# Kernel tuning notes

Measured on AMD Instinct MI355X. Metric: run time of the kernel, lower is better.

The kernel has to match this reference:

```python
import jax, jax.numpy as jnp
import numpy as np

B, L, H = 2, 2048, 1024
NH = 4
K = int(H * 0.5)       # key_dim = 512
V = int(H * 1.0)       # value_dim = 1024
DK, DV = K // NH, V // NH   # 128, 256
PR = 32                # proj_low_rank_dim
GR = 64                # gate_low_rank_dim
EPS = 1e-5


def setup_inputs() -> dict:
    key = jax.random.key(0)
    ks = jax.random.split(key, 16)
    s = 0.02
    return {
        "x": jax.random.normal(ks[0], (B, L, H), jnp.float32),
        "mu_x": jax.random.normal(ks[1], (H,), jnp.float32) * s,      # LerpLinear mu of x_proj[0]
        "Wx1": jax.random.normal(ks[2], (5 * PR, H), jnp.float32) * s,  # x_proj[0].linear
        "Wx2": jax.random.normal(ks[3], (H, 5 * PR), jnp.float32) * s,  # x_proj[2]
        "x_bias": jax.random.normal(ks[4], (5, H), jnp.float32) * s,
        "Wr": jax.random.normal(ks[5], (K, H), jnp.float32) * s,
        "Wk": jax.random.normal(ks[6], (K, H), jnp.float32) * s,
        "Wv": jax.random.normal(ks[7], (V, H), jnp.float32) * s,
        "Wg": jax.random.normal(ks[8], (V, H), jnp.float32) * s,
        "Ww1": jax.random.normal(ks[9], (GR, H), jnp.float32) * s,     # w_proj LoRA down
        "Ww2": jax.random.normal(ks[10], (K, GR), jnp.float32) * s,    # w_proj LoRA up
        "bw2": jax.random.normal(ks[11], (K,), jnp.float32) * s,
        "bonus": jax.random.normal(ks[12], (NH, DK), jnp.float32) * s,  # u
        "ln_w": jnp.ones((DV,), jnp.float32),
        "ln_b": jnp.zeros((DV,), jnp.float32),
        "Wo": jax.random.normal(ks[13], (H, V), jnp.float32) * s,
    }


def reference(x, mu_x, Wx1, Wx2, x_bias, Wr, Wk, Wv, Wg, Ww1, Ww2, bw2,
              bonus, ln_w, ln_b, Wo):
    b, l, h = x.shape
    # token shift: shifted[t] = x[t-1], zeros at t=0 (nn.ZeroPad2d((0,0,1,-1)))
    shifted = jnp.pad(x, ((0, 0), (1, 0), (0, 0)))[:, :-1]
    delta = shifted - x

    # x_proj: LerpLinear -> tanh -> einsum with o_proj-like weight, 5 mixing vectors
    xp = jnp.tanh((x + delta * mu_x) @ Wx1.T).reshape(b, l, 5, PR)
    mus = jnp.einsum('blnr,hnr->blnh', xp, Wx2.reshape(H, 5, PR)) + x_bias
    mu_r, mu_w, mu_k, mu_v, mu_g = (mus[:, :, i] for i in range(5))

    # DDLerpLinear projections: linear(x + delta * mu)
    r = (x + delta * mu_r) @ Wr.T                                   # [B,L,K]
    w = jnp.tanh((x + delta * mu_w) @ Ww1.T) @ Ww2.T + bw2          # LoRA, [B,L,K]
    k = (x + delta * mu_k) @ Wk.T                                   # [B,L,K]
    v = (x + delta * mu_v) @ Wv.T                                   # [B,L,V]
    g = (x + delta * mu_g) @ Wg.T                                   # [B,L,V]

    r = r.reshape(b, l, NH, DK)
    k = k.reshape(b, l, NH, DK)
    v = v.reshape(b, l, NH, DV)
    w = -jnp.exp(w.reshape(b, l, NH, DK))   # log-decay (negative)

    def step(S, inp):
        r_t, k_t, v_t, w_t = inp                                    # [B,h,dk]/[B,h,dv]
        kv = k_t[..., :, None] * v_t[..., None, :]                  # [B,h,dk,dv]
        o_t = jnp.einsum('bhk,bhkv->bhv', r_t,
                         S + bonus[None, :, :, None] * kv)
        S = jnp.exp(w_t)[..., None] * S + kv
        return S, o_t

    seq = (r.transpose(1, 0, 2, 3), k.transpose(1, 0, 2, 3),
           v.transpose(1, 0, 2, 3), w.transpose(1, 0, 2, 3))
    S0 = jnp.zeros((b, NH, DK, DV), x.dtype)
    _, o = jax.lax.scan(step, S0, seq)       # [L,B,h,dv]
    o = o.transpose(1, 0, 2, 3)              # [B,L,h,dv]

    # per-head LayerNorm fused with swish gate
    mean = o.mean(-1, keepdims=True)
    var = o.var(-1, keepdims=True)
    o = (o - mean) * jax.lax.rsqrt(var + EPS) * ln_w + ln_b
    gh = g.reshape(b, l, NH, DV)
    o = o * (gh * jax.nn.sigmoid(gh))        # swish gate

    return o.reshape(b, l, V) @ Wo.T         # [B,L,H]
```

## Files before the change

### kernel.cpp

```cpp
#include <hip/hip_runtime.h>
#include <cstdint>
#include <cstddef>

#define H     1024
#define LSEQ  2048
#define NHH   4
#define DKK   128
#define DVV   256
#define KDIM  512
#define VDIM  1024
#define GRR   64
#define MTOT  4096

enum { EPI_NONE = 0, EPI_TANH = 1, EPI_DEC = 3 };

typedef __attribute__((ext_vector_type(8))) _Float16 half8;
typedef __attribute__((ext_vector_type(4))) float f32x4;
typedef __attribute__((ext_vector_type(2))) float f32x2;

static __device__ __forceinline__ unsigned short f2h(float f) {
    _Float16 h = (_Float16)f;
    union { _Float16 h; unsigned short u; } c;
    c.h = h;
    return c.u;
}

template<int CTRL>
static __device__ __forceinline__ f32x2 dpp_add2(f32x2 x) {
    int lo = __builtin_amdgcn_update_dpp(0, __float_as_int(x.x), CTRL, 0xf, 0xf, true);
    int hi = __builtin_amdgcn_update_dpp(0, __float_as_int(x.y), CTRL, 0xf, 0xf, true);
    f32x2 m;
    m.x = __int_as_float(lo);
    m.y = __int_as_float(hi);
    return x + m;
}

__global__ __launch_bounds__(256) void lerp5_kernel(
    const float* __restrict__ xp,
    const float* __restrict__ Wx2,
    const float* __restrict__ xb,
    const float* __restrict__ x,
    unsigned short* __restrict__ insb)
{
    __shared__ float As[16][64];
    __shared__ float Bs[16][64];
    const int m0 = blockIdx.x * 64;
    const int n0 = blockIdx.y * 64;
    const int t  = threadIdx.x;
    const int tx = t & 15, ty = t >> 4;
    const int sm = t >> 2;
    const int sq = (t & 3) * 4;
    const int nbase = n0 + tx * 4;

    float4 xv[4], pv[4];
#pragma unroll
    for (int i = 0; i < 4; i++) {
        const int m = m0 + ty * 4 + i;
        xv[i] = *(const float4*)(x + (size_t)m * H + nbase);
        pv[i] = make_float4(0.f, 0.f, 0.f, 0.f);
        if ((m & (LSEQ - 1)) != 0)
            pv[i] = *(const float4*)(x + (size_t)(m - 1) * H + nbase);
    }

    for (int z = 0; z < 5; z++) {
        const int acol = z * 32;
        float acc[4][4];
#pragma unroll
        for (int i = 0; i < 4; i++)
#pragma unroll
            for (int j = 0; j < 4; j++) acc[i][j] = 0.f;

#pragma unroll
        for (int k0 = 0; k0 < 32; k0 += 16) {
            {
                const int m = m0 + sm;
                const float4 av = *(const float4*)(xp + (size_t)m * 256 + acol + k0 + sq);
                As[sq + 0][sm] = av.x; As[sq + 1][sm] = av.y;
                As[sq + 2][sm] = av.z; As[sq + 3][sm] = av.w;
            }
            {
                const int n = n0 + sm;
                const float4 bv = *(const float4*)(Wx2 + (size_t)n * 160 + acol + k0 + sq);
                Bs[sq + 0][sm] = bv.x; Bs[sq + 1][sm] = bv.y;
                Bs[sq + 2][sm] = bv.z; Bs[sq + 3][sm] = bv.w;
            }
            __syncthreads();
#pragma unroll
            for (int kk = 0; kk < 16; kk++) {
                const float4 a = *(const float4*)&As[kk][ty * 4];
                const float4 b = *(const float4*)&Bs[kk][tx * 4];
                const float av2[4] = {a.x, a.y, a.z, a.w};
                const float bv2[4] = {b.x, b.y, b.z, b.w};
#pragma unroll
                for (int i = 0; i < 4; i++)
#pragma unroll
                    for (int j = 0; j < 4; j++) acc[i][j] += av2[i] * bv2[j];
            }
            __syncthreads();
        }

        const float4 bb = *(const float4*)(xb + z * H + nbase);
        unsigned short* dst = insb + (size_t)z * 4194304;
#pragma unroll
        for (int i = 0; i < 4; i++) {
            const int m = m0 + ty * 4 + i;
            float4 r;
            r.x = xv[i].x + (pv[i].x - xv[i].x) * (acc[i][0] + bb.x);
            r.y = xv[i].y + (pv[i].y - xv[i].y) * (acc[i][1] + bb.y);
            r.z = xv[i].z + (pv[i].z - xv[i].z) * (acc[i][2] + bb.z);
            r.w = xv[i].w + (pv[i].w - xv[i].w) * (acc[i][3] + bb.w);
            ushort4 p;
            p.x = f2h(r.x); p.y = f2h(r.y); p.z = f2h(r.z); p.w = f2h(r.w);
            *(ushort4*)(dst + (size_t)m * H + nbase) = p;
        }
    }
}

template<int EPI>
__global__ __launch_bounds__(256) void gemm_mfma_bt(
    const unsigned short* __restrict__ A,
    const unsigned short* __restrict__ A2, int nsplit, int lda,
    const unsigned short* __restrict__ B, int ldb,
    float* __restrict__ C, unsigned short* __restrict__ Ch, int ldc, int K,
    const float* __restrict__ bias)
{
    __shared__ __align__(16) unsigned short As[128 * 32];
    __shared__ __align__(16) unsigned short Bs[128 * 32];
    const int t    = threadIdx.x;
    const int w    = t >> 6;
    const int lane = t & 63;
    const int m0 = blockIdx.x * 128;
    const int n0 = blockIdx.y * 128;
    const unsigned short* Au = (n0 < nsplit) ? A : A2;
    const int mw = (w & 1) * 64;
    const int nw = (w >> 1) * 64;
    const int l15 = lane & 15;
    const int q4  = lane >> 4;

    f32x4 acc[4][4];
#pragma unroll
    for (int i = 0; i < 4; i++)
#pragma unroll
        for (int j = 0; j < 4; j++) {
            f32x4 z = {0.f, 0.f, 0.f, 0.f};
            acc[i][j] = z;
        }

    for (int k0 = 0; k0 < K; k0 += 32) {
        __syncthreads();
#pragma unroll
        for (int jj = 0; jj < 2; jj++) {
            const int c   = w * 128 + jj * 64 + lane;
            const int row = c >> 2;
            const int col = (c & 3) * 8;
            __builtin_amdgcn_global_load_lds(
                (const __attribute__((address_space(1))) void*)(Au + (size_t)(m0 + row) * lda + k0 + col),
                (__attribute__((address_space(3))) void*)((char*)As + (w * 128 + jj * 64) * 16),
                16, 0, 0);
            __builtin_amdgcn_global_load_lds(
                (const __attribute__((address_space(1))) void*)(B + (size_t)(n0 + row) * ldb + k0 + col),
                (__attribute__((address_space(3))) void*)((char*)Bs + (w * 128 + jj * 64) * 16),
                16, 0, 0);
        }
        __syncthreads();

        half8 a[4], b[4];
#pragma unroll
        for (int i = 0; i < 4; i++)
            a[i] = *(const half8*)(As + (mw + i * 16 + l15) * 32 + q4 * 8);
#pragma unroll
        for (int j = 0; j < 4; j++)
            b[j] = *(const half8*)(Bs + (nw + j * 16 + l15) * 32 + q4 * 8);
#pragma unroll
        for (int i = 0; i < 4; i++)
#pragma unroll
            for (int j = 0; j < 4; j++)
                acc[i][j] = __builtin_amdgcn_mfma_f32_16x16x32_f16(a[i], b[j], acc[i][j], 0, 0, 0);
    }

#pragma unroll
    for (int i = 0; i < 4; i++) {
        const int m_base = m0 + mw + i * 16 + q4 * 4;
#pragma unroll
        for (int j = 0; j < 4; j++) {
            const int n = n0 + nw + j * 16 + l15;
#pragma unroll
            for (int r = 0; r < 4; r++) {
                float val = acc[i][j][r];
                if constexpr (EPI == EPI_TANH) {
                    C[(size_t)(m_base + r) * ldc + n] = tanhf(val);
                } else if constexpr (EPI == EPI_DEC) {
                    C[(size_t)(m_base + r) * ldc + n] = expf(-expf(val + bias[n]));
                } else {
                    C[(size_t)(m_base + r) * ldc + n] = val;
                }
            }
        }
    }
}

__global__ __launch_bounds__(256) void gemm_fused3(
    const unsigned short* __restrict__ s0, const unsigned short* __restrict__ s1,
    const unsigned short* __restrict__ s2, const unsigned short* __restrict__ s3,
    const unsigned short* __restrict__ s4,
    const unsigned short* __restrict__ Ww1p, const unsigned short* __restrict__ Wrb,
    const unsigned short* __restrict__ Wvb,
    unsigned short* __restrict__ wlow16, float* __restrict__ rkB,
    float* __restrict__ vgB)
{
    const int y = blockIdx.y;
    const unsigned short *Au, *Bp;
    float* C = nullptr;
    unsigned short* Ch = nullptr;
    int n0, ldc;
    if (y == 0) {
        Au = s1; Bp = Ww1p; n0 = 0; ldc = 128; Ch = wlow16;
    } else if (y <= 8) {
        n0 = (y - 1) * 128;
        Au = (n0 < 512) ? s0 : s2;
        Bp = Wrb; C = rkB; ldc = 1024;
    } else {
        n0 = (y - 9) * 128;
        Au = (n0 < 1024) ? s3 : s4;
        Bp = Wvb; C = vgB; ldc = 2048;
    }

    __shared__ __align__(16) unsigned short As[128 * 32];
    __shared__ __align__(16) unsigned short Bs[128 * 32];
    const int t    = threadIdx.x;
    const int w    = t >> 6;
    const int lane = t & 63;
    const int m0 = blockIdx.x * 128;
    const int mw = (w & 1) * 64;
    const int nw = (w >> 1) * 64;
    const int l15 = lane & 15;
    const int q4  = lane >> 4;

    f32x4 acc[4][4];
#pragma unroll
    for (int i = 0; i < 4; i++)
#pragma unroll
        for (int j = 0; j < 4; j++) {
            f32x4 z = {0.f, 0.f, 0.f, 0.f};
            acc[i][j] = z;
        }

    for (int k0 = 0; k0 < H; k0 += 32) {
        __syncthreads();
#pragma unroll
        for (int jj = 0; jj < 2; jj++) {
            const int c   = w * 128 + jj * 64 + lane;
            const int row = c >> 2;
            const int col = (c & 3) * 8;
            __builtin_amdgcn_global_load_lds(
                (const __attribute__((address_space(1))) void*)(Au + (size_t)(m0 + row) * H + k0 + col),
                (__attribute__((address_space(3))) void*)((char*)As + (w * 128 + jj * 64) * 16),
                16, 0, 0);
            __builtin_amdgcn_global_load_lds(
                (const __attribute__((address_space(1))) void*)(Bp + (size_t)(n0 + row) * H + k0 + col),
                (__attribute__((address_space(3))) void*)((char*)Bs + (w * 128 + jj * 64) * 16),
                16, 0, 0);
        }
        __syncthreads();

        half8 a[4], b[4];
#pragma unroll
        for (int i = 0; i < 4; i++)
            a[i] = *(const half8*)(As + (mw + i * 16 + l15) * 32 + q4 * 8);
#pragma unroll
        for (int j = 0; j < 4; j++)
            b[j] = *(const half8*)(Bs + (nw + j * 16 + l15) * 32 + q4 * 8);
#pragma unroll
        for (int i = 0; i < 4; i++)
#pragma unroll
            for (int j = 0; j < 4; j++)
                acc[i][j] = __builtin_amdgcn_mfma_f32_16x16x32_f16(a[i], b[j], acc[i][j], 0, 0, 0);
    }

#pragma unroll
    for (int i = 0; i < 4; i++) {
        const int m_base = m0 + mw + i * 16 + q4 * 4;
#pragma unroll
        for (int j = 0; j < 4; j++) {
            const int n = n0 + nw + j * 16 + l15;
#pragma unroll
            for (int r = 0; r < 4; r++) {
                float val = acc[i][j][r];
                if (Ch) Ch[(size_t)(m_base + r) * ldc + n] = f2h(tanhf(val));
                else    C[(size_t)(m_base + r) * ldc + n] = val;
            }
        }
    }
}

__global__ __launch_bounds__(256) void gemm_mfma_corr(
    const unsigned short* __restrict__ rt16,
    const unsigned short* __restrict__ SentryT16,
    float* __restrict__ o, int segl)
{
    const int z   = blockIdx.z;
    const int seg = (z >> 3) + 1;
    const int bh  = z & 7;
    const int b   = bh >> 2, h = bh & 3;
    const unsigned short* A = rt16 + ((size_t)b * LSEQ + (size_t)seg * segl) * KDIM + h * DKK;
    const unsigned short* B = SentryT16 + (size_t)(seg * 8 + bh) * 32768;
    float* C = o + ((size_t)b * LSEQ + (size_t)seg * segl) * VDIM + h * DVV;

    __shared__ __align__(16) unsigned short As[128 * 32];
    __shared__ __align__(16) unsigned short Bs[128 * 32];
    const int t    = threadIdx.x;
    const int w    = t >> 6;
    const int lane = t & 63;
    const int m0 = blockIdx.x * 128;
    const int n0 = blockIdx.y * 128;
    const int mw = (w & 1) * 64;
    const int nw = (w >> 1) * 64;
    const int l15 = lane & 15;
    const int q4  = lane >> 4;

    f32x4 acc[4][4];
#pragma unroll
    for (int i = 0; i < 4; i++)
#pragma unroll
        for (int j = 0; j < 4; j++) {
            f32x4 zz = {0.f, 0.f, 0.f, 0.f};
            acc[i][j] = zz;
        }

    for (int k0 = 0; k0 < 128; k0 += 32) {
        __syncthreads();
#pragma unroll
        for (int jj = 0; jj < 2; jj++) {
            const int c   = w * 128 + jj * 64 + lane;
            const int row = c >> 2;
            const int col = (c & 3) * 8;
            __builtin_amdgcn_global_load_lds(
                (const __attribute__((address_space(1))) void*)(A + (size_t)(m0 + row) * KDIM + k0 + col),
                (__attribute__((address_space(3))) void*)((char*)As + (w * 128 + jj * 64) * 16),
                16, 0, 0);
            __builtin_amdgcn_global_load_lds(
                (const __attribute__((address_space(1))) void*)(B + (size_t)(n0 + row) * 128 + k0 + col),
                (__attribute__((address_space(3))) void*)((char*)Bs + (w * 128 + jj * 64) * 16),
                16, 0, 0);
        }
        __syncthreads();

        half8 a[4], bb[4];
#pragma unroll
        for (int i = 0; i < 4; i++)
            a[i] = *(const half8*)(As + (mw + i * 16 + l15) * 32 + q4 * 8);
#pragma unroll
        for (int j = 0; j < 4; j++)
            bb[j] = *(const half8*)(Bs + (nw + j * 16 + l15) * 32 + q4 * 8);
#pragma unroll
        for (int i = 0; i < 4; i++)
#pragma unroll
            for (int j = 0; j < 4; j++)
                acc[i][j] = __builtin_amdgcn_mfma_f32_16x16x32_f16(a[i], bb[j], acc[i][j], 0, 0, 0);
    }

#pragma unroll
    for (int i = 0; i < 4; i++) {
        const int mrow = mw + i * 16 + q4 * 4;
        const int m_base = m0 + mrow;
#pragma unroll
        for (int j = 0; j < 4; j++) {
            const int n = n0 + nw + j * 16 + l15;
#pragma unroll
            for (int rr = 0; rr < 4; rr++)
                if (mrow + rr < segl)
                    C[(size_t)(m_base + rr) * VDIM + n] += acc[i][j][rr];
        }
    }
}

__global__ __launch_bounds__(256) void prep_kernel(
    const float* __restrict__ Wr, const float* __restrict__ Wk,
    const float* __restrict__ Wv, const float* __restrict__ Wg,
    const float* __restrict__ Wo, const float* __restrict__ Wx1,
    const float* __restrict__ Ww1, const float* __restrict__ Ww2,
    unsigned short* __restrict__ Wb, unsigned short* __restrict__ Wx1p,
    unsigned short* __restrict__ Ww1p, unsigned short* __restrict__ Ww2p,
    const float* __restrict__ x, const float* __restrict__ mux,
    unsigned short* __restrict__ xl16)
{
    const int bx = blockIdx.x;
    if (bx < 4512) {
        const int q = bx * 256 + threadIdx.x;
        float4 v = make_float4(0.f, 0.f, 0.f, 0.f);
        unsigned short* dst;
        if (q < 1048576) {
            const int i4 = q * 4;
            const float* src; int off;
            if      (i4 <  524288) { src = Wr; off = i4; }
            else if (i4 < 1048576) { src = Wk; off = i4 -  524288; }
            else if (i4 < 2097152) { src = Wv; off = i4 - 1048576; }
            else if (i4 < 3145728) { src = Wg; off = i4 - 2097152; }
            else                   { src = Wo; off = i4 - 3145728; }
            v = *(const float4*)(src + off);
            dst = Wb + i4;
        } else if (q < 1114112) {
            const int e = (q - 1048576) * 4;
            const int row = e >> 10;
            if (row < 160) v = *(const float4*)(Wx1 + (size_t)row * H + (e & 1023));
            dst = Wx1p + e;
        } else if (q < 1146880) {
            const int e = (q - 1114112) * 4;
            const int row = e >> 10;
            if (row < 64) v = *(const float4*)(Ww1 + (size_t)row * H + (e & 1023));
            dst = Ww1p + e;
        } else {
            const int e = (q - 1146880) * 4;
            v = *(const float4*)(Ww2 + e);
            dst = Ww2p + e;
        }
        ushort4 o4;
        o4.x = f2h(v.x); o4.y = f2h(v.y); o4.z = f2h(v.z); o4.w = f2h(v.w);
        *(ushort4*)dst = o4;
    } else {
        const int m = bx - 4512;
        const int c = threadIdx.x * 4;
        const float4 xv = *(const float4*)(x + (size_t)m * H + c);
        float4 pv = make_float4(0.f, 0.f, 0.f, 0.f);
        if ((m & (LSEQ - 1)) != 0)
            pv = *(const float4*)(x + (size_t)(m - 1) * H + c);
        const float4 mv = *(const float4*)(mux + c);
        ushort4 p;
        p.x = f2h(xv.x + (pv.x - xv.x) * mv.x);
        p.y = f2h(xv.y + (pv.y - xv.y) * mv.y);
        p.z = f2h(xv.z + (pv.z - xv.z) * mv.z);
        p.w = f2h(xv.w + (pv.w - xv.w) * mv.w);
        *(ushort4*)(xl16 + (size_t)m * H + c) = p;
    }
}

template<int SEGL_T>
__global__ __launch_bounds__(256, 4) void scan_pass1(
    const float* __restrict__ rk, const float* __restrict__ vg,
    const float* __restrict__ dec, const float* __restrict__ bonus,
    float* __restrict__ o, unsigned short* __restrict__ rt16,
    float* __restrict__ Sloc, float* __restrict__ Dtot)
{
    const int bh  = blockIdx.x & 7;
    const int vc  = (blockIdx.x >> 3) & 7;
    const int seg = blockIdx.x >> 6;
    const int b   = bh >> 2;
    const int h   = bh & 3;
    const int t   = threadIdx.x;
    const int kg  = t & 31;
    const int vl  = t >> 5;
    const bool wlead = (vc == 0) && (vl == 0);

    f32x2 S2[4][2];
    float D[4] = {1.f, 1.f, 1.f, 1.f}, u[4];
#pragma unroll
    for (int j = 0; j < 4; j++) {
        u[j] = bonus[h * DKK + kg * 4 + j];
        f32x2 z = {0.f, 0.f};
        S2[j][0] = z; S2[j][1] = z;
    }

    const size_t row0 = (size_t)b * LSEQ + (size_t)seg * SEGL_T;
    const float* rp = rk  + row0 * 1024 + h * DKK + kg * 4;
    const float* dp = dec + row0 * 512  + h * DKK + kg * 4;
    const float* vp = vg  + row0 * 2048 + h * DVV + vc * 32 + vl * 4;
    float*       op = o   + row0 * 1024 + h * DVV + vc * 32 + vl * 4;
    unsigned short* rt = rt16 + row0 * 512 + h * DKK + kg * 4;

    float4 cr = *(const float4*)rp;
    float4 ck = *(const float4*)(rp + 512);
    float4 cd = *(const float4*)dp;
    float4 cv = *(const float4*)vp;
    rp += 1024; dp += 512; vp += 2048;

#pragma unroll 2
    for (int t0 = 0; t0 < SEGL_T; ++t0) {
        const float4 nr = *(const float4*)rp;
        const float4 nk = *(const float4*)(rp + 512);
        const float4 nd = *(const float4*)dp;
        const float4 nv = *(const float4*)vp;
        rp += 1024; dp += 512; vp += 2048;

        if (wlead) {
            ushort4 p;
            p.x = f2h(cr.x * D[0]); p.y = f2h(cr.y * D[1]);
            p.z = f2h(cr.z * D[2]); p.w = f2h(cr.w * D[3]);
            *(ushort4*)rt = p;
        }
        rt += 512;

        const float ra[4] = {cr.x, cr.y, cr.z, cr.w};
        const float ka[4] = {ck.x, ck.y, ck.z, ck.w};
        const float da[4] = {cd.x, cd.y, cd.z, cd.w};
        f32x2 va2[2];
        va2[0].x = cv.x; va2[0].y = cv.y;
        va2[1].x = cv.z; va2[1].y = cv.w;
        f32x2 part2[2];
        part2[0] = (f32x2){0.f, 0.f};
        part2[1] = (f32x2){0.f, 0.f};
#pragma unroll
        for (int j = 0; j < 4; j++) {
#pragma unroll
            for (int p = 0; p < 2; p++) {
                const f32x2 kv2 = va2[p] * ka[j];
                part2[p] += ra[j] * (S2[j][p] + u[j] * kv2);
                S2[j][p] = da[j] * S2[j][p] + kv2;
            }
            D[j] *= da[j];
        }
#pragma unroll
        for (int p = 0; p < 2; p++) {
            part2[p] = dpp_add2<0xB1>(part2[p]);
            part2[p] = dpp_add2<0x4E>(part2[p]);
            part2[p] = dpp_add2<0x141>(part2[p]);
            part2[p] = dpp_add2<0x140>(part2[p]);
            part2[p] = dpp_add2<0x142>(part2[p]);
        }
        if (kg == 31) {
            float4 res = make_float4(part2[0].x, part2[0].y, part2[1].x, part2[1].y);
            *(float4*)op = res;
        }
        op += 1024;
        cr = nr; ck = nk; cd = nd; cv = nv;
    }

    {
        float* sl = Sloc + (size_t)(seg * 8 + bh) * 32768
                    + (size_t)(kg * 4) * 256 + vc * 32 + vl * 4;
#pragma unroll
        for (int j = 0; j < 4; j++) {
            float4 sv = make_float4(S2[j][0].x, S2[j][0].y, S2[j][1].x, S2[j][1].y);
            *(float4*)(sl + j * 256) = sv;
        }
        if (wlead) {
            float* dt = Dtot + (seg * 8 + bh) * 128 + kg * 4;
#pragma unroll
            for (int j = 0; j < 4; j++) dt[j] = D[j];
        }
    }
}

__global__ __launch_bounds__(256) void scan_pass2(
    const float* __restrict__ Sloc, const float* __restrict__ Dtot,
    unsigned short* __restrict__ SentryT16, int nseg)
{
    const int vc = blockIdx.x & 31;
    const int bh = blockIdx.x >> 5;
    const int t  = threadIdx.x;
    const int kg = t & 31;
    const int vl = t >> 5;

    float S[4] = {0.f, 0.f, 0.f, 0.f};
    for (int p = 0; p < nseg; p++) {
        unsigned short* st = SentryT16 + (size_t)(p * 8 + bh) * 32768
                             + (size_t)(vc * 8 + vl) * 128 + kg * 4;
        ushort4 pk;
        pk.x = f2h(S[0]); pk.y = f2h(S[1]); pk.z = f2h(S[2]); pk.w = f2h(S[3]);
        *(ushort4*)st = pk;
        if (p < nseg - 1) {
            const float* sl = Sloc + (size_t)(p * 8 + bh) * 32768
                              + (size_t)(kg * 4) * 256 + vc * 8 + vl;
            const float* dt = Dtot + (p * 8 + bh) * 128 + kg * 4;
#pragma unroll
            for (int j = 0; j < 4; j++) S[j] = dt[j] * S[j] + sl[j * 256];
        }
    }
}

__global__ __launch_bounds__(256) void ln_gate_kernel(
    const float* __restrict__ o, const float* __restrict__ vg,
    const float* __restrict__ lnw, const float* __restrict__ lnb,
    unsigned short* __restrict__ out)
{
    const int m    = blockIdx.x;
    const int t    = threadIdx.x;
    const int h    = t >> 6;
    const int lane = t & 63;
    const size_t obase = (size_t)m * VDIM + (size_t)h * DVV + lane * 4;
    const size_t gbase = (size_t)m * 2048 + 1024 + (size_t)h * DVV + lane * 4;
    const float4 ov = *(const float4*)(o + obase);
    float sum = ov.x + ov.y + ov.z + ov.w;
    float sq  = ov.x * ov.x + ov.y * ov.y + ov.z * ov.z + ov.w * ov.w;
#pragma unroll
    for (int off = 1; off < 64; off <<= 1) {
        sum += __shfl_xor(sum, off);
        sq  += __shfl_xor(sq, off);
    }
    const float mean = sum * (1.f / DVV);
    const float var  = sq * (1.f / DVV) - mean * mean;
    const float rstd = rsqrtf(var + 1e-5f);
    const float4 gv = *(const float4*)(vg + gbase);
    const float4 wv = *(const float4*)(lnw + lane * 4);
    const float4 bv = *(const float4*)(lnb + lane * 4);
    float4 res;
    res.x = ((ov.x - mean) * rstd * wv.x + bv.x) * (gv.x / (1.f + expf(-gv.x)));
    res.y = ((ov.y - mean) * rstd * wv.y + bv.y) * (gv.y / (1.f + expf(-gv.y)));
    res.z = ((ov.z - mean) * rstd * wv.z + bv.z) * (gv.z / (1.f + expf(-gv.z)));
    res.w = ((ov.w - mean) * rstd * wv.w + bv.w) * (gv.w / (1.f + expf(-gv.w)));
    ushort4 p;
    p.x = f2h(res.x); p.y = f2h(res.y); p.z = f2h(res.z); p.w = f2h(res.w);
    *(ushort4*)(out + obase) = p;
}

extern "C" void kernel_launch(void* const* d_in, const int* in_sizes, int n_in,
                              void* d_out, int out_size, void* d_ws, size_t ws_size,
                              hipStream_t stream)
{
    const float* x     = (const float*)d_in[0];
    const float* mu_x  = (const float*)d_in[1];
    const float* Wx1   = (const float*)d_in[2];
    const float* Wx2   = (const float*)d_in[3];
    const float* xb    = (const float*)d_in[4];
    const float* Wr    = (const float*)d_in[5];
    const float* Wk    = (const float*)d_in[6];
    const float* Wv    = (const float*)d_in[7];
    const float* Wg    = (const float*)d_in[8];
    const float* Ww1   = (const float*)d_in[9];
    const float* Ww2   = (const float*)d_in[10];
    const float* bw2   = (const float*)d_in[11];
    const float* bonus = (const float*)d_in[12];
    const float* lnw   = (const float*)d_in[13];
    const float* lnb   = (const float*)d_in[14];
    const float* Wo    = (const float*)d_in[15];
    float* out = (float*)d_out;
    (void)in_sizes; (void)n_in; (void)out_size;

    float* ws = (float*)d_ws;
    unsigned short* Wx1p = (unsigned short*)(ws + 0);
    unsigned short* Ww1p = (unsigned short*)(ws + 131072);
    unsigned short* Ww2p = (unsigned short*)(ws + 196608);
    unsigned short* Wb   = (unsigned short*)(ws + 212992);
    float* xp     = ws + 2310144;
    unsigned short* wlow16 = (unsigned short*)(ws + 3358720);
    float* insB   = ws + 3620864;
    float* rkB    = ws + 14106624;
    float* vgB    = ws + 18301952;
    float* decB   = ws + 26692608;

    unsigned short* insb = (unsigned short*)insB;
    unsigned short* Wrb  = Wb;
    unsigned short* Wvb  = Wb + 1048576;
    unsigned short* Wob  = Wb + 3145728;
    unsigned short* xl16 = (unsigned short*)rkB;
    float*          o       = insB;
    unsigned short* rt16    = insb + 2ul * 4194304;
    float*          Dtot    = (float*)wlow16;
    unsigned short* gatedb  = (unsigned short*)(insB + 3ul * 2097152);

    const size_t need32 = 41373184ull * sizeof(float);
    const int  nseg = (ws_size >= need32) ? 32 : 16;
    const int  segl = LSEQ / nseg;
    float* Sloc = (nseg == 32) ? (ws + 28790272)
                               : (insB + 3ul * 2097152);
    unsigned short* SentryT16 = (nseg == 32) ? (unsigned short*)(ws + 37178880)
                                             : (unsigned short*)decB;

    dim3 blk(256);

    prep_kernel<<<dim3(8608), blk, 0, stream>>>(Wr, Wk, Wv, Wg, Wo, Wx1, Ww1, Ww2,
                                                Wb, Wx1p, Ww1p, Ww2p, x, mu_x, xl16);

    gemm_mfma_bt<EPI_TANH><<<dim3(32, 2), blk, 0, stream>>>(
        xl16, xl16, 1 << 30, H, Wx1p, H, xp, nullptr, 256, H, nullptr);

    lerp5_kernel<<<dim3(64, 16), blk, 0, stream>>>(xp, Wx2, xb, x, insb);

    gemm_fused3<<<dim3(32, 25), blk, 0, stream>>>(
        insb + 0ul * 4194304, insb + 1ul * 4194304, insb + 2ul * 4194304,
        insb + 3ul * 4194304, insb + 4ul * 4194304,
        Ww1p, Wrb, Wvb, wlow16, rkB, vgB);

    gemm_mfma_bt<EPI_DEC><<<dim3(32, 4), blk, 0, stream>>>(
        wlow16, wlow16, 1 << 30, 128, Ww2p, 64, decB, nullptr, KDIM, 64, bw2);

    if (nseg == 32)
        scan_pass1<64><<<dim3(2048), blk, 0, stream>>>(rkB, vgB, decB, bonus,
                                                       o, rt16, Sloc, Dtot);
    else
        scan_pass1<128><<<dim3(1024), blk, 0, stream>>>(rkB, vgB, decB, bonus,
                                                        o, rt16, Sloc, Dtot);
    scan_pass2<<<dim3(256), blk, 0, stream>>>(Sloc, Dtot, SentryT16, nseg);
    gemm_mfma_corr<<<dim3(1, 2, (nseg - 1) * 8), blk, 0, stream>>>(
        rt16, SentryT16, o, segl);

    ln_gate_kernel<<<dim3(4096), blk, 0, stream>>>(o, vgB, lnw, lnb, gatedb);

    gemm_mfma_bt<EPI_NONE><<<dim3(32, 8), blk, 0, stream>>>(
        gatedb, gatedb, 1 << 30, VDIM, Wob, VDIM, out, nullptr, H, VDIM, nullptr);
}
```

Before: 427.3 us.

## Use packed FMA in scan inner loop and fix scan to 16 segments

The per-step state update in the chunked scan is rewritten as explicit packed float2 FMAs with broadcast scalars, so the compiler can emit packed FMA instructions instead of separate multiply and add. The host also drops the workspace-size check and always runs the 16-segment scan configuration with 128-step segments, reusing existing buffers for the local states and entry states. This gives fewer blocks and a shorter correction GEMM grid, but each scan block runs a longer sequential segment. If the workspace was previously large enough, this moves the default away from 32 segments.

```diff
diff --git a/kernel.cpp b/kernel.cpp
--- a/kernel.cpp
+++ b/kernel.cpp
@@ -23,6 +23,13 @@
     union { _Float16 h; unsigned short u; } c;
     c.h = h;
     return c.u;
+}
+
+static __device__ __forceinline__ f32x2 pk_fma(f32x2 a, f32x2 b, f32x2 c) {
+    return __builtin_elementwise_fma(a, b, c);
+}
+static __device__ __forceinline__ f32x2 bcast2(float s) {
+    f32x2 r; r.x = s; r.y = s; return r;
 }
 
 template<int CTRL>
@@ -500,11 +507,16 @@
         part2[1] = (f32x2){0.f, 0.f};
 #pragma unroll
         for (int j = 0; j < 4; j++) {
+            const f32x2 ka2 = bcast2(ka[j]);
+            const f32x2 ra2 = bcast2(ra[j]);
+            const f32x2 da2 = bcast2(da[j]);
+            const f32x2 u2  = bcast2(u[j]);
 #pragma unroll
             for (int p = 0; p < 2; p++) {
-                const f32x2 kv2 = va2[p] * ka[j];
-                part2[p] += ra[j] * (S2[j][p] + u[j] * kv2);
-                S2[j][p] = da[j] * S2[j][p] + kv2;
+                const f32x2 kv2 = va2[p] * ka2;
+                const f32x2 su  = pk_fma(u2, kv2, S2[j][p]);
+                part2[p]        = pk_fma(ra2, su, part2[p]);
+                S2[j][p]        = pk_fma(da2, S2[j][p], kv2);
             }
             D[j] *= da[j];
         }
@@ -623,7 +635,7 @@
     const float* lnb   = (const float*)d_in[14];
     const float* Wo    = (const float*)d_in[15];
     float* out = (float*)d_out;
-    (void)in_sizes; (void)n_in; (void)out_size;
+    (void)in_sizes; (void)n_in; (void)out_size; (void)ws_size;
 
     float* ws = (float*)d_ws;
     unsigned short* Wx1p = (unsigned short*)(ws + 0);
@@ -644,16 +656,13 @@
     unsigned short* xl16 = (unsigned short*)rkB;
     float*          o       = insB;
     unsigned short* rt16    = insb + 2ul * 4194304;
+    float*          Sloc    = insB + 3ul * 2097152;
     float*          Dtot    = (float*)wlow16;
+    unsigned short* SentryT16 = (unsigned short*)decB;
     unsigned short* gatedb  = (unsigned short*)(insB + 3ul * 2097152);
 
-    const size_t need32 = 41373184ull * sizeof(float);
-    const int  nseg = (ws_size >= need32) ? 32 : 16;
-    const int  segl = LSEQ / nseg;
-    float* Sloc = (nseg == 32) ? (ws + 28790272)
-                               : (insB + 3ul * 2097152);
-    unsigned short* SentryT16 = (nseg == 32) ? (unsigned short*)(ws + 37178880)
-                                             : (unsigned short*)decB;
+    const int nseg = 16;
+    const int segl = LSEQ / nseg;
 
     dim3 blk(256);
 
@@ -673,12 +682,8 @@
     gemm_mfma_bt<EPI_DEC><<<dim3(32, 4), blk, 0, stream>>>(
         wlow16, wlow16, 1 << 30, 128, Ww2p, 64, decB, nullptr, KDIM, 64, bw2);
 
-    if (nseg == 32)
-        scan_pass1<64><<<dim3(2048), blk, 0, stream>>>(rkB, vgB, decB, bonus,
-                                                       o, rt16, Sloc, Dtot);
-    else
-        scan_pass1<128><<<dim3(1024), blk, 0, stream>>>(rkB, vgB, decB, bonus,
-                                                        o, rt16, Sloc, Dtot);
+    scan_pass1<128><<<dim3(1024), blk, 0, stream>>>(rkB, vgB, decB, bonus,
+                                                    o, rt16, Sloc, Dtot);
     scan_pass2<<<dim3(256), blk, 0, stream>>>(Sloc, Dtot, SentryT16, nseg);
     gemm_mfma_corr<<<dim3(1, 2, (nseg - 1) * 8), blk, 0, stream>>>(
         rt16, SentryT16, o, segl);
```

Result: faster. 396.0 us (-7.3%).
